# Performance work log

Hardware: AMD Instinct MI355X
Metric: run time of the kernel (lower is better)

The kernel has to match this reference:

```python
import jax, jax.numpy as jnp
import numpy as np

GROUPS = 32
EPS = 1e-5


def _group_norm(x, scale, bias):
    B, C, H, W = x.shape
    xg = x.reshape(B, GROUPS, -1)
    mu = xg.mean(axis=-1, keepdims=True)
    var = jnp.mean(jnp.square(xg - mu), axis=-1, keepdims=True)
    xn = ((xg - mu) * jax.lax.rsqrt(var + EPS)).reshape(B, C, H, W)
    return xn * scale[None, :, None, None] + bias[None, :, None, None]


def _conv1x1(x, w, b):
    # x: [B,C,H,W], w: [O,C], b: [O]
    return jnp.einsum('bchw,oc->bohw', x, w) + b[None, :, None, None]


def setup_inputs() -> dict:
    key = jax.random.key(0)
    ks = jax.random.split(key, 6)
    B, C, H, W = 16, 512, 32, 32
    x = jax.random.normal(ks[0], (B, C, H, W), dtype=jnp.float32)
    # xavier_uniform for [C, C, 1, 1] conv: limit = sqrt(6 / (fan_in + fan_out)) = sqrt(6 / (2C))
    lim = float(np.sqrt(6.0 / (2 * C)))
    wq = jax.random.uniform(ks[1], (C, C), jnp.float32, -lim, lim)
    wk = jax.random.uniform(ks[2], (C, C), jnp.float32, -lim, lim)
    wv = jax.random.uniform(ks[3], (C, C), jnp.float32, -lim, lim)
    wo = jax.random.uniform(ks[4], (C, C), jnp.float32, -lim, lim) * 1e-5  # gain=1e-5
    zeros_c = jnp.zeros((C,), jnp.float32)
    return {
        'x': x,
        'gn_scale': jnp.ones((C,), jnp.float32),
        'gn_bias': zeros_c,
        'wq': wq, 'bq': zeros_c,
        'wk': wk, 'bk': zeros_c,
        'wv': wv, 'bv': zeros_c,
        'wo': wo, 'bo': zeros_c,
    }


def reference(x, gn_scale, gn_bias, wq, bq, wk, bk, wv, bv, wo, bo):
    B, C, H, W = x.shape
    N = H * W
    h = _group_norm(x, gn_scale, gn_bias)
    q = _conv1x1(h, wq, bq).reshape(B, C, N)  # [B,C,N]
    k = _conv1x1(h, wk, bk).reshape(B, C, N)
    v = _conv1x1(h, wv, bv).reshape(B, C, N)
    scale = 1.0 / jnp.sqrt(jnp.asarray(C, x.dtype))
    w = jnp.einsum('bcn,bcm->bnm', q, k) * scale  # [B,N,N]
    w = jax.nn.softmax(w, axis=-1)
    hv = jnp.einsum('bnm,bcm->bcn', w, v).reshape(B, C, H, W)
    out = _conv1x1(hv, wo, bo)
    return x + out
```

## Files before the change

kernel.cpp:

```cpp
#include <hip/hip_runtime.h>
#include <hip/hip_bf16.h>
#include <cstdint>

typedef unsigned char u8;
typedef float floatx4 __attribute__((ext_vector_type(4)));
typedef int intx8 __attribute__((ext_vector_type(8)));

__device__ __forceinline__ void gld_lds16(const void* g, void* l) {
    __builtin_amdgcn_global_load_lds(
        (const __attribute__((address_space(1))) unsigned int*)g,
        (__attribute__((address_space(3))) unsigned int*)l, 16, 0, 0);
}

__device__ __forceinline__ u8 f2fp8(float v) {
    return (u8)(__builtin_amdgcn_cvt_pk_fp8_f32(v, v, 0, false) & 0xff);
}
__device__ __forceinline__ unsigned int pack4_fp8(float a, float b, float c, float d) {
    unsigned int u = __builtin_amdgcn_cvt_pk_fp8_f32(a, b, 0, false);
    u = __builtin_amdgcn_cvt_pk_fp8_f32(c, d, u, true);
    return u;
}

__device__ __forceinline__ intx8 ld_frag(const u8* p, int lo, int hi) {
    uint4 a = *(const uint4*)(p + lo);
    uint4 b = *(const uint4*)(p + hi);
    intx8 r;
    r[0] = a.x; r[1] = a.y; r[2] = a.z; r[3] = a.w;
    r[4] = b.x; r[5] = b.y; r[6] = b.z; r[7] = b.w;
    return r;
}
__device__ __forceinline__ intx8 ld_frag_g(const u8* p) {
    uint4 a = *(const uint4*)(p);
    uint4 b = *(const uint4*)(p + 16);
    intx8 r;
    r[0] = a.x; r[1] = a.y; r[2] = a.z; r[3] = a.w;
    r[4] = b.x; r[5] = b.y; r[6] = b.z; r[7] = b.w;
    return r;
}


__global__ __launch_bounds__(256) void setup_kernel(
    const float* __restrict__ x, const float* __restrict__ gs,
    const float* __restrict__ gb,
    const float* __restrict__ wq, const float* __restrict__ wk,
    const float* __restrict__ wv, const float* __restrict__ wo,
    const float* __restrict__ bq, const float* __restrict__ bk,
    const float* __restrict__ bv,
    u8* __restrict__ hT, u8* __restrict__ wqkv, u8* __restrict__ wob,
    float* __restrict__ bqkv)
{
    const int t = threadIdx.x;
    if (blockIdx.x >= 512) {
        int i = (blockIdx.x - 512) * 256 + t;
        if (i < 786432) {
            int which = i >> 18;
            int off = i & 262143;
            const float* src = which == 0 ? wq : which == 1 ? wk : wv;
            wqkv[i] = f2fp8(src[off]);
        } else {
            wob[i - 786432] = f2fp8(wo[i - 786432] * 262144.0f);
        }
        if (i < 1536)
            bqkv[i] = i < 512 ? bq[i] : (i < 1024 ? bk[i - 512] : bv[i - 1024]);
        return;
    }
    const int b = blockIdx.x >> 5;
    const int g = blockIdx.x & 31;
    const int wave = t >> 6, lane = t & 63;
    const float4* x4 = (const float4*)(x + ((long long)b * 512 + g * 16) * 1024);

    float4 v[16];
    float s1 = 0.f, s2 = 0.f;
#pragma unroll
    for (int i = 0; i < 16; ++i) {
        v[i] = x4[i * 256 + t];
        s1 += v[i].x + v[i].y + v[i].z + v[i].w;
        s2 += v[i].x * v[i].x + v[i].y * v[i].y + v[i].z * v[i].z + v[i].w * v[i].w;
    }
#pragma unroll
    for (int m = 32; m; m >>= 1) {
        s1 += __shfl_xor(s1, m, 64);
        s2 += __shfl_xor(s2, m, 64);
    }
    __shared__ float red[2][4];
    __shared__ float stats[2];
    if (lane == 0) { red[0][wave] = s1; red[1][wave] = s2; }
    __syncthreads();
    if (t == 0) {
        float a = red[0][0] + red[0][1] + red[0][2] + red[0][3];
        float q = red[1][0] + red[1][1] + red[1][2] + red[1][3];
        float mu = a * (1.0f / 16384.0f);
        float var = q * (1.0f / 16384.0f) - mu * mu;
        stats[0] = mu;
        stats[1] = rsqrtf(var + 1e-5f);
    }
    __syncthreads();
    const float mu = stats[0], rs = stats[1];

#pragma unroll
    for (int i = 0; i < 16; ++i) {
        const float sc = gs[g * 16 + i] * rs;
        const float bi = gb[g * 16 + i] - mu * sc;
        v[i].x = v[i].x * sc + bi;
        v[i].y = v[i].y * sc + bi;
        v[i].z = v[i].z * sc + bi;
        v[i].w = v[i].w * sc + bi;
    }
    u8* hb = hT + (long long)b * 524288 + g * 16;
#pragma unroll
    for (int r = 0; r < 4; ++r) {
        uint4 o;
        o.x = pack4_fp8(v[0][r],  v[1][r],  v[2][r],  v[3][r]);
        o.y = pack4_fp8(v[4][r],  v[5][r],  v[6][r],  v[7][r]);
        o.z = pack4_fp8(v[8][r],  v[9][r],  v[10][r], v[11][r]);
        o.w = pack4_fp8(v[12][r], v[13][r], v[14][r], v[15][r]);
        *(uint4*)(hb + (long long)(4 * t + r) * 512) = o;
    }
}

template <int EPI>
__global__ __launch_bounds__(256, 3) void gemm_mx(
    const u8* __restrict__ A, long long sA,
    const u8* __restrict__ B, long long sB,
    void* __restrict__ C, long long sC,
    void* __restrict__ C2, void* __restrict__ C3,
    int ldC, int K,
    const float* __restrict__ bias,
    const float* __restrict__ resid, long long sR,
    float scale)
{
    __shared__ __align__(16) u8 smem[33792];
    const int tid = threadIdx.x;
    const int l = tid & 63;
    const int wave = tid >> 6;
    const int wm = wave >> 1, wn = wave & 1;
    const int bm = blockIdx.x, bn = blockIdx.y, b = blockIdx.z;

    const u8* Ab = A + (long long)b * sA + (long long)bm * 128 * K;
    const u8* Bb = B + (long long)b * sB + (long long)bn * 128 * K;

    const int srow = wave * 8 + (l >> 3);
    const int sg = ((l & 7) ^ ((l >> 3) & 7)) * 16;
    const u8* ga  = Ab + (long long)srow * K + sg;
    const u8* gbp = Bb + (long long)srow * K + sg;
    const long long c32 = (long long)32 * K;
    const int ldst = wave * 1024;

    const int q4 = l >> 4;
    const int ln = l & 15;
    const int glo = ((2 * q4) ^ (l & 7)) * 16;
    const int ghi = ((2 * q4 + 1) ^ (l & 7)) * 16;
    int arow[4], brow[4];
#pragma unroll
    for (int i = 0; i < 4; ++i) {
        arow[i] = (wm * 64 + i * 16 + ln) * 128;
        brow[i] = (wn * 64 + i * 16 + ln) * 128 + 16384;
    }

    floatx4 acc[4][4] = {};
    const int niter = K >> 7;

    for (int it = 0; it < niter; ++it) {
        const int k0 = it << 7;
#pragma unroll
        for (int c = 0; c < 4; ++c) {
            gld_lds16(ga + c * c32 + k0, smem + c * 4096 + ldst);
            gld_lds16(gbp + c * c32 + k0, smem + 16384 + c * 4096 + ldst);
        }
        __syncthreads();
        intx8 bfr[4];
#pragma unroll
        for (int j = 0; j < 4; ++j) bfr[j] = ld_frag(smem + brow[j], glo, ghi);
#pragma unroll
        for (int i = 0; i < 4; ++i) {
            intx8 af = ld_frag(smem + arow[i], glo, ghi);
#pragma unroll
            for (int j = 0; j < 4; ++j)
                acc[i][j] = __builtin_amdgcn_mfma_scale_f32_16x16x128_f8f6f4(
                    af, bfr[j], acc[i][j], 0, 0, 0, 127, 0, 127);
        }
        __syncthreads();
    }

    if (EPI == 3) {
        float* Cf = (float*)C;
        float* lf = (float*)smem;
#pragma unroll
        for (int h = 0; h < 2; ++h) {
            if (wm == h) {
#pragma unroll
                for (int i = 0; i < 4; ++i) {
#pragma unroll
                    for (int j = 0; j < 4; ++j) {
                        const int cl = wn * 64 + j * 16 + ln;
#pragma unroll
                        for (int r = 0; r < 4; ++r) {
                            const int rl = i * 16 + q4 * 4 + r;
                            lf[rl * 132 + cl] = acc[i][j][r] * scale
                                + bias[bm * 128 + h * 64 + rl];
                        }
                    }
                }
            }
            __syncthreads();
#pragma unroll
            for (int it = 0; it < 8; ++it) {
                const int rl = it * 8 + (tid >> 5);
                const int c4 = (tid & 31) * 4;
                const long long gro = (long long)b * sR
                    + (long long)(bm * 128 + h * 64 + rl) * ldC + bn * 128 + c4;
                float4 vv = *(const float4*)(lf + rl * 132 + c4);
                const float4 rr = *(const float4*)(resid + gro);
                vv.x += rr.x; vv.y += rr.y; vv.z += rr.z; vv.w += rr.w;
                *(float4*)(Cf + (long long)b * sC
                    + (long long)(bm * 128 + h * 64 + rl) * ldC + bn * 128 + c4) = vv;
            }
            __syncthreads();
        }
    } else if (EPI == 1) {
        const int which = bn >> 2;
        u8* tile = smem;
#pragma unroll
        for (int i = 0; i < 4; ++i) {
            const int rl = wm * 64 + i * 16 + q4 * 4;
#pragma unroll
            for (int j = 0; j < 4; ++j) {
                const int cl = wn * 64 + j * 16 + ln;
                const float badd = bias[bn * 128 + cl];
                if (which == 2) {
                    *(unsigned int*)(tile + cl * 144 + rl) =
                        pack4_fp8(acc[i][j][0] + badd, acc[i][j][1] + badd,
                                  acc[i][j][2] + badd, acc[i][j][3] + badd);
                } else {
#pragma unroll
                    for (int r = 0; r < 4; ++r)
                        tile[(rl + r) * 144 + cl] = f2fp8(acc[i][j][r] + badd);
                }
            }
        }
        __syncthreads();
        const int w2  = wave >> 1;
        const int cbl = (wave & 1) * 2 + (l >> 5);
        const int lnw = (l >> 1) & 15;
        const int g16 = (l & 1) * 16;
#pragma unroll
        for (int p = 0; p < 4; ++p) {
            const int rtile = p * 2 + w2;
            uint4 dd = *(const uint4*)(tile + (rtile * 16 + lnw) * 144 + cbl * 32 + g16);
            u8* dst;
            if (which == 0)
                dst = (u8*)C + (long long)b * sC + (long long)(bm * 8 + rtile) * 8192
                      + ((bn & 3) * 4 + cbl) * 512 + lnw * 32 + g16;
            else if (which == 1)
                dst = (u8*)C2 + (long long)b * sC + (long long)(bm * 8 + rtile) * 8192
                      + ((bn & 3) * 4 + cbl) * 512 + lnw * 32 + g16;
            else
                dst = (u8*)C3 + (long long)b * sC + (long long)((bn & 3) * 8 + rtile) * 16384
                      + (long long)(bm * 4 + cbl) * 512 + lnw * 32 + g16;
            *(uint4*)dst = dd;
        }
    }
}

__global__ __launch_bounds__(256, 2) void attn_core(
    const u8* __restrict__ qg, const u8* __restrict__ kg,
    const u8* __restrict__ vg, u8* __restrict__ hvT)
{
    __shared__ __align__(16) u8 smem[8704];
    const int tid = threadIdx.x;
    const int l = tid & 63;
    const int w = tid >> 6;
    const int d = blockIdx.x;
    const int b  = (d & 7) * 2 + ((d >> 8) & 1);
    const int bq = (d >> 3) & 31;

    const u8* qb = qg + (long long)b * 524288 + (long long)(bq * 2) * 8192;
    const u8* kb = kg + (long long)b * 524288;
    const u8* vb = vg + (long long)b * 524288;

    const int q4 = l >> 4;
    const int ln = l & 15;
    const int glo = ((2 * q4) ^ (l & 7)) * 16;
    const int ghi = ((2 * q4 + 1) ^ (l & 7)) * 16;
    const int lo32 = ln * 32;

    intx8 qf[2][4];
#pragma unroll
    for (int j = 0; j < 2; ++j)
#pragma unroll
        for (int kc = 0; kc < 4; ++kc)
            qf[j][kc] = ld_frag_g(qb + j * 8192 + (kc * 4 + q4) * 512 + lo32);

    floatx4 acc_pv[8][2] = {};
    float psum[2] = {0.f, 0.f};
    const float scale = 0.044194173824159216f;

    for (int mt = 0; mt < 8; ++mt) {
        u8* E = smem + (mt & 1) * 4096;
        floatx4 acc_s[2][2] = {};
#pragma unroll
        for (int kc = 0; kc < 4; ++kc) {
#pragma unroll
            for (int i = 0; i < 2; ++i) {
                intx8 kf = ld_frag_g(kb + (long long)(mt * 8 + w * 2 + i) * 8192
                                        + (kc * 4 + q4) * 512 + lo32);
#pragma unroll
                for (int j = 0; j < 2; ++j)
                    acc_s[i][j] = __builtin_amdgcn_mfma_scale_f32_16x16x128_f8f6f4(
                        kf, qf[j][kc], acc_s[i][j], 0, 0, 0, 127, 0, 127);
            }
        }
        intx8 vfA[4], vfB[4];
        const u8* vrow = vb + (long long)(w * 8) * 16384 + (mt * 4 + q4) * 512 + lo32;
#pragma unroll
        for (int i = 0; i < 4; ++i)
            vfA[i] = ld_frag_g(vrow + (long long)i * 16384);
#pragma unroll
        for (int i = 0; i < 2; ++i) {
#pragma unroll
            for (int j = 0; j < 2; ++j) {
                float e0 = __expf(acc_s[i][j][0] * scale);
                float e1 = __expf(acc_s[i][j][1] * scale);
                float e2 = __expf(acc_s[i][j][2] * scale);
                float e3 = __expf(acc_s[i][j][3] * scale);
                psum[j] += e0 + e1 + e2 + e3;
                const int n = j * 16 + ln;
                const int m0 = w * 32 + i * 16 + q4 * 4;
                *(unsigned int*)(E + n * 128 + (m0 ^ ((n & 7) * 16))) =
                    pack4_fp8(e0 * 0.25f, e1 * 0.25f, e2 * 0.25f, e3 * 0.25f);
            }
        }
        __syncthreads();
#pragma unroll
        for (int i = 0; i < 4; ++i)
            vfB[i] = ld_frag_g(vrow + (long long)(i + 4) * 16384);
        intx8 ef[2];
#pragma unroll
        for (int j = 0; j < 2; ++j)
            ef[j] = ld_frag(E + (j * 16 + ln) * 128, glo, ghi);
#pragma unroll
        for (int i = 0; i < 4; ++i)
#pragma unroll
            for (int j = 0; j < 2; ++j)
                acc_pv[i][j] = __builtin_amdgcn_mfma_scale_f32_16x16x128_f8f6f4(
                    vfA[i], ef[j], acc_pv[i][j], 0, 0, 0, 127, 0, 127);
#pragma unroll
        for (int i = 0; i < 4; ++i)
#pragma unroll
            for (int j = 0; j < 2; ++j)
                acc_pv[i + 4][j] = __builtin_amdgcn_mfma_scale_f32_16x16x128_f8f6f4(
                    vfB[i], ef[j], acc_pv[i + 4][j], 0, 0, 0, 127, 0, 127);
    }

#pragma unroll
    for (int j = 0; j < 2; ++j) {
        psum[j] += __shfl_xor(psum[j], 16, 64);
        psum[j] += __shfl_xor(psum[j], 32, 64);
    }
    float* sb = (float*)(smem + 8192);
    if (l < 16) {
        sb[w * 32 + l]      = psum[0];
        sb[w * 32 + 16 + l] = psum[1];
    }
    __syncthreads();
    float rln[2];
#pragma unroll
    for (int j = 0; j < 2; ++j) {
        const int n = j * 16 + ln;
        rln[j] = 4.0f / (sb[n] + sb[32 + n] + sb[64 + n] + sb[96 + n]);
    }
    u8* ob = hvT + (long long)b * 524288 + (long long)(bq * 32) * 512;
#pragma unroll
    for (int i = 0; i < 8; ++i) {
#pragma unroll
        for (int j = 0; j < 2; ++j) {
            const int n = j * 16 + ln;
            const int c = w * 128 + i * 16 + q4 * 4;
            *(unsigned int*)(ob + (long long)n * 512 + c) =
                pack4_fp8(acc_pv[i][j][0] * rln[j], acc_pv[i][j][1] * rln[j],
                          acc_pv[i][j][2] * rln[j], acc_pv[i][j][3] * rln[j]);
        }
    }
}

extern "C" void kernel_launch(void* const* d_in, const int* in_sizes, int n_in,
                              void* d_out, int out_size, void* d_ws, size_t ws_size,
                              hipStream_t stream)
{
    const float* x  = (const float*)d_in[0];
    const float* gs = (const float*)d_in[1];
    const float* gb = (const float*)d_in[2];
    const float* wq = (const float*)d_in[3];
    const float* bq = (const float*)d_in[4];
    const float* wk = (const float*)d_in[5];
    const float* bk = (const float*)d_in[6];
    const float* wv = (const float*)d_in[7];
    const float* bv = (const float*)d_in[8];
    const float* wo = (const float*)d_in[9];
    const float* bo = (const float*)d_in[10];
    float* out = (float*)d_out;

    u8* p = (u8*)d_ws;
    u8* hT   = p; p += 8388608;
    u8* q    = p; p += 8388608;
    u8* k    = p; p += 8388608;
    u8* v    = p; p += 8388608;
    u8* wqkv = p; p += 786432;
    float* bqkv = (float*)p; p += 6144;
    u8* wob  = p; p += 262144;
    u8* hvT  = p; p += 8388608;

    setup_kernel<<<4608, 256, 0, stream>>>(x, gs, gb, wq, wk, wv, wo, bq, bk, bv,
                                           hT, wqkv, wob, bqkv);

    gemm_mx<1><<<dim3(8, 12, 16), 256, 0, stream>>>(
        hT, 524288LL, wqkv, 0LL, q, 524288LL, k, v,
        512, 512, bqkv, nullptr, 0LL, 1.0f);

    attn_core<<<dim3(512, 1, 1), 256, 0, stream>>>(q, k, v, hvT);

    gemm_mx<3><<<dim3(4, 8, 16), 256, 0, stream>>>(
        wob, 0LL, hvT, 524288LL, out, 524288LL, nullptr, nullptr,
        1024, 512, bo, x, 524288LL, 3.814697265625e-06f);
}
```

Baseline: 173.6 us.

## Fuse output projection and residual add into attention kernel

Folds the final 1x1 output convolution, bias and residual add into the attention kernel's epilogue. Each block stages its normalized PV tile in swizzled shared memory and multiplies it by a pre-tiled fp8 Wo read directly from global memory. This removes a kernel launch and the fp8 hvT round trip through global memory. In exchange, shared memory per block grows, every block re-reads all of Wo, and the fp32 output stores are strided per channel rather than coalesced through shared memory.

Result: faster. 170.1 us (-2.0%).

```diff
diff --git a/kernel.cpp b/kernel.cpp
--- a/kernel.cpp
+++ b/kernel.cpp
@@ -58,7 +58,10 @@
             const float* src = which == 0 ? wq : which == 1 ? wk : wv;
             wqkv[i] = f2fp8(src[off]);
         } else {
-            wob[i - 786432] = f2fp8(wo[i - 786432] * 262144.0f);
+            int i2 = i - 786432;
+            int row = i2 >> 9, col = i2 & 511;
+            wob[(long long)(row >> 4) * 8192 + (col >> 5) * 512
+                + (row & 15) * 32 + (col & 31)] = f2fp8(wo[i2] * 262144.0f);
         }
         if (i < 1536)
             bqkv[i] = i < 512 ? bq[i] : (i < 1024 ? bk[i - 512] : bv[i - 1024]);
@@ -125,9 +128,7 @@
     void* __restrict__ C, long long sC,
     void* __restrict__ C2, void* __restrict__ C3,
     int ldC, int K,
-    const float* __restrict__ bias,
-    const float* __restrict__ resid, long long sR,
-    float scale)
+    const float* __restrict__ bias)
 {
     __shared__ __align__(16) u8 smem[33792];
     const int tid = threadIdx.x;
@@ -182,42 +183,7 @@
         __syncthreads();
     }
 
-    if (EPI == 3) {
-        float* Cf = (float*)C;
-        float* lf = (float*)smem;
-#pragma unroll
-        for (int h = 0; h < 2; ++h) {
-            if (wm == h) {
-#pragma unroll
-                for (int i = 0; i < 4; ++i) {
-#pragma unroll
-                    for (int j = 0; j < 4; ++j) {
-                        const int cl = wn * 64 + j * 16 + ln;
-#pragma unroll
-                        for (int r = 0; r < 4; ++r) {
-                            const int rl = i * 16 + q4 * 4 + r;
-                            lf[rl * 132 + cl] = acc[i][j][r] * scale
-                                + bias[bm * 128 + h * 64 + rl];
-                        }
-                    }
-                }
-            }
-            __syncthreads();
-#pragma unroll
-            for (int it = 0; it < 8; ++it) {
-                const int rl = it * 8 + (tid >> 5);
-                const int c4 = (tid & 31) * 4;
-                const long long gro = (long long)b * sR
-                    + (long long)(bm * 128 + h * 64 + rl) * ldC + bn * 128 + c4;
-                float4 vv = *(const float4*)(lf + rl * 132 + c4);
-                const float4 rr = *(const float4*)(resid + gro);
-                vv.x += rr.x; vv.y += rr.y; vv.z += rr.z; vv.w += rr.w;
-                *(float4*)(Cf + (long long)b * sC
-                    + (long long)(bm * 128 + h * 64 + rl) * ldC + bn * 128 + c4) = vv;
-            }
-            __syncthreads();
-        }
-    } else if (EPI == 1) {
+    {
         const int which = bn >> 2;
         u8* tile = smem;
 #pragma unroll
@@ -262,11 +228,13 @@
     }
 }
 
-__global__ __launch_bounds__(256, 2) void attn_core(
+__global__ __launch_bounds__(256, 2) void attn_out(
     const u8* __restrict__ qg, const u8* __restrict__ kg,
-    const u8* __restrict__ vg, u8* __restrict__ hvT)
+    const u8* __restrict__ vg, const u8* __restrict__ wot,
+    const float* __restrict__ bo, const float* __restrict__ xg,
+    float* __restrict__ outg)
 {
-    __shared__ __align__(16) u8 smem[8704];
+    __shared__ __align__(16) u8 smem[25088];
     const int tid = threadIdx.x;
     const int l = tid & 63;
     const int w = tid >> 6;
@@ -369,16 +337,55 @@
         const int n = j * 16 + ln;
         rln[j] = 4.0f / (sb[n] + sb[32 + n] + sb[64 + n] + sb[96 + n]);
     }
-    u8* ob = hvT + (long long)b * 524288 + (long long)(bq * 32) * 512;
+
+    u8* HV = smem + 8704;
 #pragma unroll
     for (int i = 0; i < 8; ++i) {
 #pragma unroll
         for (int j = 0; j < 2; ++j) {
             const int n = j * 16 + ln;
-            const int c = w * 128 + i * 16 + q4 * 4;
-            *(unsigned int*)(ob + (long long)n * 512 + c) =
+            const int m0 = i * 16 + q4 * 4;
+            *(unsigned int*)(HV + w * 4096 + n * 128 + (m0 ^ ((n & 7) * 16))) =
                 pack4_fp8(acc_pv[i][j][0] * rln[j], acc_pv[i][j][1] * rln[j],
                           acc_pv[i][j][2] * rln[j], acc_pv[i][j][3] * rln[j]);
+        }
+    }
+    __syncthreads();
+
+    floatx4 acc2[8][2] = {};
+#pragma unroll
+    for (int kc = 0; kc < 4; ++kc) {
+        intx8 hvf[2];
+#pragma unroll
+        for (int j = 0; j < 2; ++j)
+            hvf[j] = ld_frag(HV + kc * 4096 + (j * 16 + ln) * 128, glo, ghi);
+#pragma unroll
+        for (int rb = 0; rb < 8; ++rb) {
+            intx8 wof = ld_frag_g(wot + (long long)(w * 8 + rb) * 8192
+                                      + (kc * 4 + q4) * 512 + lo32);
+#pragma unroll
+            for (int j = 0; j < 2; ++j)
+                acc2[rb][j] = __builtin_amdgcn_mfma_scale_f32_16x16x128_f8f6f4(
+                    wof, hvf[j], acc2[rb][j], 0, 0, 0, 127, 0, 127);
+        }
+    }
+
+    const float osc = 3.814697265625e-06f;
+    const float* xb = xg + (long long)b * 524288;
+    float* og = outg + (long long)b * 524288;
+    const int n0 = bq * 32;
+#pragma unroll
+    for (int rb = 0; rb < 8; ++rb) {
+        const int oc0 = w * 128 + rb * 16 + q4 * 4;
+#pragma unroll
+        for (int j = 0; j < 2; ++j) {
+            const int n = n0 + j * 16 + ln;
+#pragma unroll
+            for (int r = 0; r < 4; ++r) {
+                const int oc = oc0 + r;
+                og[(long long)oc * 1024 + n] =
+                    acc2[rb][j][r] * osc + bo[oc] + xb[(long long)oc * 1024 + n];
+            }
         }
     }
 }
@@ -408,18 +415,13 @@
     u8* wqkv = p; p += 786432;
     float* bqkv = (float*)p; p += 6144;
     u8* wob  = p; p += 262144;
-    u8* hvT  = p; p += 8388608;
 
     setup_kernel<<<4608, 256, 0, stream>>>(x, gs, gb, wq, wk, wv, wo, bq, bk, bv,
                                            hT, wqkv, wob, bqkv);
 
     gemm_mx<1><<<dim3(8, 12, 16), 256, 0, stream>>>(
         hT, 524288LL, wqkv, 0LL, q, 524288LL, k, v,
-        512, 512, bqkv, nullptr, 0LL, 1.0f);
-
-    attn_core<<<dim3(512, 1, 1), 256, 0, stream>>>(q, k, v, hvT);
-
-    gemm_mx<3><<<dim3(4, 8, 16), 256, 0, stream>>>(
-        wob, 0LL, hvT, 524288LL, out, 524288LL, nullptr, nullptr,
-        1024, 512, bo, x, 524288LL, 3.814697265625e-06f);
-}
+        512, 512, bqkv);
+
+    attn_out<<<dim3(512, 1, 1), 256, 0, stream>>>(q, k, v, wob, bo, x, out);
+}
```
